# Performance work log

Measured on AMD Instinct MI355X. Metric: run time of the kernel, lower is better.

## Reference

```python
import jax, jax.numpy as jnp
import numpy as np
from jax import lax

T, LC = 4096, 20           # sentence length, max word length in chars
CV, CE, CO = 100, 25, 25   # char vocab, char emb dim, char-cnn out channels
V, E = 100000, 512         # word vocab, word emb dim
H = 1024                   # lstm hidden size per direction
NT, START, STOP = 12, 10, 11
NEG = -10000.0


def _lstm_dir(x, w_ih, w_hh, b_ih, b_hh):
    # x: [T, In] -> hs: [T, H]; pytorch gate order i, f, g, o
    pre = x @ w_ih.T + (b_ih + b_hh)              # [T, 4H] (input part hoisted out of scan)
    h0 = jnp.zeros((H,), x.dtype)
    def step(carry, p):
        h, c = carry
        g = p + h @ w_hh.T
        i, f, gg, o = jnp.split(g, 4)
        i = jax.nn.sigmoid(i); f = jax.nn.sigmoid(f)
        gg = jnp.tanh(gg); o = jax.nn.sigmoid(o)
        c = f * c + i * gg
        h = o * jnp.tanh(c)
        return (h, c), h
    _, hs = lax.scan(step, (h0, h0), pre)
    return hs


def _features(sentence, chars, char_emb, cnn_w, cnn_b, word_emb,
              w_ih_f, w_hh_f, b_ih_f, b_hh_f, w_ih_b, w_hh_b, b_ih_b, b_hh_b,
              w_tag, b_tag):
    # char CNN: embed -> conv2d(kernel (3,CE), pad (2,0)) -> max-pool over full time axis
    ce = char_emb[chars][:, None, :, :]            # [T,1,LC,CE]
    y = lax.conv_general_dilated(ce, cnn_w, (1, 1), ((2, 2), (0, 0)),
                                 dimension_numbers=('NCHW', 'OIHW', 'NCHW'))
    y = y + cnn_b[None, :, None, None]             # [T,CO,LC+2,1]
    char_feat = y.max(axis=(2, 3))                 # [T,CO]
    emb = jnp.concatenate([word_emb[sentence], char_feat], axis=1)  # [T,E+CO]
    # dropout is identity in eval mode
    hf = _lstm_dir(emb, w_ih_f, w_hh_f, b_ih_f, b_hh_f)
    hb = _lstm_dir(emb[::-1], w_ih_b, w_hh_b, b_ih_b, b_hh_b)[::-1]
    out = jnp.concatenate([hf, hb], axis=1)        # [T,2H]
    return out @ w_tag.T + b_tag                   # [T,NT]


def _viterbi(feats, transitions):
    alpha0 = jnp.full((NT,), NEG, feats.dtype).at[START].set(0.0)
    def step(alpha, feat):
        smat = alpha[:, None] + feat[None, :] + transitions   # [from, to]
        return jax.nn.logsumexp(smat, axis=0), jnp.argmax(smat, axis=0)
    alpha, bptrs = lax.scan(step, alpha0, feats)               # bptrs: [T,NT]
    final = alpha + transitions[:, STOP]                       # [NT]
    score = jax.nn.logsumexp(final)
    best_last = jnp.argmax(final)
    def back(best, b):
        nb = b[best]
        return nb, nb
    _, prev = lax.scan(back, best_last, bptrs[1:][::-1])
    path = jnp.concatenate([prev[::-1], best_last[None]])      # [T]
    return score, path


def setup_inputs() -> dict:
    key = jax.random.key(0)
    ks = jax.random.split(key, 18)
    IN = E + CO
    tr = jax.random.normal(ks[17], (NT, NT), jnp.float32)
    tr = tr.at[:, START].set(NEG).at[STOP, :].set(NEG)
    return {
        'sentence': jax.random.randint(ks[0], (T,), 0, V),
        'chars': jax.random.randint(ks[1], (T, LC), 0, CV),
        'caps': jax.random.randint(ks[2], (T,), 0, 4),
        'char_emb': jax.random.normal(ks[3], (CV, CE), jnp.float32),
        'cnn_w': jax.random.normal(ks[4], (CO, 1, 3, CE), jnp.float32) * 0.1,
        'cnn_b': jax.random.normal(ks[5], (CO,), jnp.float32) * 0.1,
        'word_emb': jax.random.normal(ks[6], (V, E), jnp.float32),
        'w_ih_f': jax.random.normal(ks[7], (4 * H, IN), jnp.float32) * 0.02,
        'w_hh_f': jax.random.normal(ks[8], (4 * H, H), jnp.float32) * 0.02,
        'b_ih_f': jax.random.normal(ks[9], (4 * H,), jnp.float32) * 0.02,
        'b_hh_f': jax.random.normal(ks[10], (4 * H,), jnp.float32) * 0.02,
        'w_ih_b': jax.random.normal(ks[11], (4 * H, IN), jnp.float32) * 0.02,
        'w_hh_b': jax.random.normal(ks[12], (4 * H, H), jnp.float32) * 0.02,
        'b_ih_b': jax.random.normal(ks[13], (4 * H,), jnp.float32) * 0.02,
        'b_hh_b': jax.random.normal(ks[14], (4 * H,), jnp.float32) * 0.02,
        'w_tag': jax.random.normal(ks[15], (NT, 2 * H), jnp.float32) * 0.02,
        'b_tag': jax.random.normal(ks[16], (NT,), jnp.float32) * 0.02,
        'transitions': tr,
    }


def reference(sentence, chars, caps, char_emb, cnn_w, cnn_b, word_emb,
              w_ih_f, w_hh_f, b_ih_f, b_hh_f, w_ih_b, w_hh_b, b_ih_b, b_hh_b,
              w_tag, b_tag, transitions):
    # caps is accepted by the original forward signature but never used
    feats = _features(sentence, chars, char_emb, cnn_w, cnn_b, word_emb,
                      w_ih_f, w_hh_f, b_ih_f, b_hh_f, w_ih_b, w_hh_b,
                      b_ih_b, b_hh_b, w_tag, b_tag)
    return _viterbi(feats, transitions)
```

## Files before the change

### kernel.cpp

```cpp
#include <hip/hip_runtime.h>
#include <math.h>


#define T_LEN 4096
#define NTAG 12
#define START_TAG 10
#define STOP_TAG 11
#define NEG_VAL (-10000.0f)

typedef int   v4i __attribute__((ext_vector_type(4)));
typedef float v4f __attribute__((ext_vector_type(4)));
typedef short sh8 __attribute__((ext_vector_type(8)));
typedef float f32x4 __attribute__((ext_vector_type(4)));

#define OF_EMB  0UL
#define OF_W    (OF_EMB + 4096UL * 544UL)
#define OF_BIAS (OF_W + 8192UL * 544UL)
#define OF_PRE  (OF_BIAS + 8192UL)
#define OF_HF   (OF_PRE + 4096UL * 8192UL)
#define OF_HB   (OF_HF + 4097UL * 1024UL)
#define OF_FEAT (OF_HB + 4097UL * 1024UL)

__device__ __forceinline__ float fsig(float v) {
    return 1.0f / (1.0f + __expf(-v));
}
__device__ __forceinline__ float ftanhf(float v) {
    float a = fabsf(v);
    float e = __expf(-2.0f * a);
    float r = (1.0f - e) / (1.0f + e);
    return copysignf(r, v);
}
__device__ __forceinline__ unsigned f2bf(float x) {
    unsigned u = __float_as_uint(x);
    u += 0x7fffu + ((u >> 16) & 1u);
    return u >> 16;
}

__global__ void prep_w_kernel(const float* __restrict__ wf, const float* __restrict__ wb,
                              const float* __restrict__ bif, const float* __restrict__ bhf,
                              const float* __restrict__ bib, const float* __restrict__ bhb,
                              unsigned short* __restrict__ wbf, float* __restrict__ bias) {
    int n = blockIdx.x;
    const float* src = (n < 4096) ? (wf + (size_t)n * 537) : (wb + (size_t)(n - 4096) * 537);
    unsigned short* dst = wbf + (size_t)n * 544;
    for (int k = threadIdx.x; k < 544; k += blockDim.x)
        dst[k] = (k < 537) ? (unsigned short)f2bf(src[k]) : (unsigned short)0;
    if (threadIdx.x == 0)
        bias[n] = (n < 4096) ? (bif[n] + bhf[n]) : (bib[n - 4096] + bhb[n - 4096]);
}

__global__ void charcnn_kernel(const int* __restrict__ sentence, const int* __restrict__ chars,
                               const float* __restrict__ cemb, const float* __restrict__ cw,
                               const float* __restrict__ cb, const float* __restrict__ wemb,
                               unsigned short* __restrict__ emb) {
    int t = blockIdx.x, tid = threadIdx.x;
    __shared__ float ce[500];
    __shared__ float yv[550];
    for (int i = tid; i < 500; i += 256) {
        int c = chars[t * 20 + i / 25];
        ce[i] = cemb[c * 25 + i % 25];
    }
    __syncthreads();
    for (int i = tid; i < 550; i += 256) {
        int o = i / 22, p = i % 22;
        float v = cb[o];
        #pragma unroll
        for (int kh = 0; kh < 3; ++kh) {
            int ir = p - 2 + kh;
            if (ir >= 0 && ir < 20) {
                const float* crow = ce + ir * 25;
                const float* wrow = cw + o * 75 + kh * 25;
                #pragma unroll
                for (int kw = 0; kw < 25; ++kw) v = fmaf(crow[kw], wrow[kw], v);
            }
        }
        yv[o * 22 + p] = v;
    }
    __syncthreads();
    unsigned short* erow = emb + (size_t)t * 544;
    int sidx = sentence[t];
    if (tid < 128) {
        float4 v = ((const float4*)(wemb + (size_t)sidx * 512))[tid];
        uint2 pk;
        pk.x = f2bf(v.x) | (f2bf(v.y) << 16);
        pk.y = f2bf(v.z) | (f2bf(v.w) << 16);
        ((uint2*)erow)[tid] = pk;
    }
    if (tid >= 128 && tid < 153) {
        int o = tid - 128;
        const float* yo = yv + o * 22;
        float m = yo[0];
        #pragma unroll
        for (int p = 1; p < 22; ++p) m = fmaxf(m, yo[p]);
        erow[512 + o] = (unsigned short)f2bf(m);
    }
    if (tid >= 160 && tid < 167) erow[537 + (tid - 160)] = 0;
}

__global__ __launch_bounds__(256) void sgemm_kernel(const unsigned short* __restrict__ A,
                                                    const unsigned short* __restrict__ B,
                                                    const float* __restrict__ bias,
                                                    float* __restrict__ C) {
    __shared__ unsigned short As[128 * 40];
    __shared__ unsigned short Bs[128 * 40];
    const int tid = threadIdx.x;
    const int wv = tid >> 6, lane = tid & 63;
    const int l15 = lane & 15, l4 = lane >> 4;
    const int m0 = blockIdx.y * 128, n0 = blockIdx.x * 128;
    const int srow = tid >> 2, sslot = tid & 3;

    f32x4 acc[2][8];
    #pragma unroll
    for (int mt = 0; mt < 2; ++mt)
        #pragma unroll
        for (int nt = 0; nt < 8; ++nt) acc[mt][nt] = (f32x4){0.f, 0.f, 0.f, 0.f};

    for (int kt = 0; kt < 17; ++kt) {
        const int kof = kt * 32 + sslot * 8;
        uint4 a0 = *(const uint4*)(A + (size_t)(m0 + srow) * 544 + kof);
        uint4 a1 = *(const uint4*)(A + (size_t)(m0 + 64 + srow) * 544 + kof);
        uint4 b0 = *(const uint4*)(B + (size_t)(n0 + srow) * 544 + kof);
        uint4 b1 = *(const uint4*)(B + (size_t)(n0 + 64 + srow) * 544 + kof);
        __syncthreads();
        *(uint4*)&As[srow * 40 + sslot * 8] = a0;
        *(uint4*)&As[(64 + srow) * 40 + sslot * 8] = a1;
        *(uint4*)&Bs[srow * 40 + sslot * 8] = b0;
        *(uint4*)&Bs[(64 + srow) * 40 + sslot * 8] = b1;
        __syncthreads();
        sh8 bfr[8];
        #pragma unroll
        for (int nt = 0; nt < 8; ++nt)
            bfr[nt] = *(const sh8*)&Bs[(16 * nt + l15) * 40 + l4 * 8];
        #pragma unroll
        for (int mt = 0; mt < 2; ++mt) {
            sh8 afr = *(const sh8*)&As[(32 * wv + 16 * mt + l15) * 40 + l4 * 8];
            #pragma unroll
            for (int nt = 0; nt < 8; ++nt)
                acc[mt][nt] = __builtin_amdgcn_mfma_f32_16x16x32_bf16(
                    afr, bfr[nt], acc[mt][nt], 0, 0, 0);
        }
    }
    #pragma unroll
    for (int mt = 0; mt < 2; ++mt) {
        int mrow = m0 + 32 * wv + 16 * mt + l4 * 4;
        #pragma unroll
        for (int nt = 0; nt < 8; ++nt) {
            int col = n0 + 16 * nt + l15;
            float bz = bias[col];
            #pragma unroll
            for (int r = 0; r < 4; ++r)
                C[(size_t)(mrow + r) * 8192 + col] = acc[mt][nt][r] + bz;
        }
    }
}

__global__ __launch_bounds__(512, 2) void lstm_kernel(const float* __restrict__ whhf,
                                                      const float* __restrict__ whhb,
                                                      const float* __restrict__ pre,
                                                      float* __restrict__ hfbuf,
                                                      float* __restrict__ hbbuf) {
    const int tid = threadIdx.x;
    const int dir = blockIdx.x >> 6;
    const int widx = blockIdx.x & 63;
    const int j0 = widx * 16;
    const int c32 = tid >> 4;
    const int r4 = tid & 15;
    const int lane = tid & 63;
    const int wv = tid >> 6;
    const bool pol = (r4 < 8);
    __shared__ __align__(16) float partials[2][8][64];

    v4f w[4][8];
    #pragma unroll
    for (int i = 0; i < 4; ++i) {
        int R = 4 * r4 + i;
        const v4f* wsrc = (const v4f*)((dir ? whhb : whhf) +
            (size_t)(((R >> 4) << 10) + j0 + (R & 15)) * 1024 + c32 * 32);
        #pragma unroll
        for (int m = 0; m < 8; ++m) w[i][m] = wsrc[m];
    }
    #pragma unroll
    for (int i = 0; i < 4; ++i)
        #pragma unroll
        for (int m = 0; m < 8; ++m)
            asm volatile("" : "+v"(w[i][m]));

    float* hbuf = dir ? hbbuf : hfbuf;
    const int dirofs = dir ? 4096 : 0;
    float c = 0.f;

    for (int s = 0; s < T_LEN; ++s) {
        const int t = dir ? (T_LEN - 1 - s) : s;
        const int rdslot = dir ? (t + 1) : t;
        const int wrslot = dir ? t : (t + 1);
        const int p = s & 1;

        float preg = 0.f;
        if (tid < 64)
            preg = pre[(size_t)t * 8192 + dirofs + ((lane & 3) << 10) + j0 + (lane >> 2)];

        const float* hp = hbuf + ((size_t)rdslot << 10) + c32 * 32 + r4 * 4;
        v4i hq;
        hq.x = 0; hq.y = 0; hq.z = 0; hq.w = 0;
        if (pol) {
            asm volatile("global_load_dwordx4 %0, %1, off sc1\n\ts_waitcnt vmcnt(0)"
                         : "=v"(hq) : "v"(hp));
        }
        while (true) {
            bool miss = pol && (hq.x == -1 || hq.y == -1 || hq.z == -1 || hq.w == -1);
            if (!__any(miss)) break;
            __builtin_amdgcn_s_sleep(1);
            if (miss) {
                asm volatile("global_load_dwordx4 %0, %1, off sc1\n\ts_waitcnt vmcnt(0)"
                             : "=v"(hq) : "v"(hp));
            }
        }

        float a0 = 0.f, a1 = 0.f, a2 = 0.f, a3 = 0.f;
        #pragma unroll
        for (int m = 0; m < 8; ++m) {
            int src = (lane & 48) + m;
            float hx = __shfl(__int_as_float(hq.x), src);
            float hy = __shfl(__int_as_float(hq.y), src);
            float hz = __shfl(__int_as_float(hq.z), src);
            float hw = __shfl(__int_as_float(hq.w), src);
            a0 = fmaf(w[0][m].x, hx, a0); a0 = fmaf(w[0][m].y, hy, a0);
            a0 = fmaf(w[0][m].z, hz, a0); a0 = fmaf(w[0][m].w, hw, a0);
            a1 = fmaf(w[1][m].x, hx, a1); a1 = fmaf(w[1][m].y, hy, a1);
            a1 = fmaf(w[1][m].z, hz, a1); a1 = fmaf(w[1][m].w, hw, a1);
            a2 = fmaf(w[2][m].x, hx, a2); a2 = fmaf(w[2][m].y, hy, a2);
            a2 = fmaf(w[2][m].z, hz, a2); a2 = fmaf(w[2][m].w, hw, a2);
            a3 = fmaf(w[3][m].x, hx, a3); a3 = fmaf(w[3][m].y, hy, a3);
            a3 = fmaf(w[3][m].z, hz, a3); a3 = fmaf(w[3][m].w, hw, a3);
        }
        a0 += __shfl_xor(a0, 16); a0 += __shfl_xor(a0, 32);
        a1 += __shfl_xor(a1, 16); a1 += __shfl_xor(a1, 32);
        a2 += __shfl_xor(a2, 16); a2 += __shfl_xor(a2, 32);
        a3 += __shfl_xor(a3, 16); a3 += __shfl_xor(a3, 32);
        if ((lane >> 4) == 0)
            *(float4*)&partials[p][wv][r4 << 2] = make_float4(a0, a1, a2, a3);
        __syncthreads();

        if (tid < 64) {
            int rql = ((lane & 3) << 4) + (lane >> 2);
            float dsum = 0.f;
            #pragma unroll
            for (int q = 0; q < 8; ++q) dsum += partials[p][q][rql];
            float val = preg + dsum;
            float act = ((lane & 3) == 2) ? ftanhf(val) : fsig(val);
            int base = lane & ~3;
            float iv = __shfl(act, base);
            float fv = __shfl(act, base + 1);
            float gv = __shfl(act, base + 2);
            float ov = __shfl(act, base + 3);
            c = fv * c + iv * gv;
            float h = ov * ftanhf(c);
            v4f hv;
            hv.x = __shfl(h, (lane << 4) & 63);
            hv.y = __shfl(h, ((lane << 4) + 4) & 63);
            hv.z = __shfl(h, ((lane << 4) + 8) & 63);
            hv.w = __shfl(h, ((lane << 4) + 12) & 63);
            if (lane < 4) {
                float* hp2 = hbuf + ((size_t)wrslot << 10) + j0 + (lane << 2);
                asm volatile("global_store_dwordx4 %0, %1, off sc1"
                             :: "v"(hp2), "v"(hv));
            }
        }
    }
}

__global__ __launch_bounds__(192) void tagproj_kernel(const float* __restrict__ hfbuf,
                                                      const float* __restrict__ hbbuf,
                                                      const float* __restrict__ wtag,
                                                      const float* __restrict__ btag,
                                                      float* __restrict__ feats) {
    int t = blockIdx.x, tid = threadIdx.x;
    __shared__ float4 hs4[512];
    for (int i = tid; i < 512; i += 192) {
        float4 q = (i < 256)
            ? ((const float4*)(hfbuf + ((size_t)(t + 1) << 10)))[i]
            : ((const float4*)(hbbuf + ((size_t)t << 10)))[i - 256];
        hs4[i ^ ((i >> 5) & 7)] = q;
    }
    __syncthreads();
    int tag = tid >> 4, sl = tid & 15;
    const float4* wrow4 = (const float4*)(wtag + (size_t)tag * 2048 + (sl << 7));
    float a = 0.f;
    #pragma unroll
    for (int m = 0; m < 32; ++m) {
        float4 h4 = hs4[(sl << 5) + (m ^ (sl & 7))];
        float4 w4 = wrow4[m];
        a = fmaf(h4.x, w4.x, a);
        a = fmaf(h4.y, w4.y, a);
        a = fmaf(h4.z, w4.z, a);
        a = fmaf(h4.w, w4.w, a);
    }
    a += __shfl_xor(a, 1);
    a += __shfl_xor(a, 2);
    a += __shfl_xor(a, 4);
    a += __shfl_xor(a, 8);
    if (sl == 0) feats[t * 12 + tag] = a + btag[tag];
}

__global__ __launch_bounds__(64) void viterbi_kernel(const float* __restrict__ feats,
                                                     const float* __restrict__ trans,
                                                     float* __restrict__ out) {
    const int tid = threadIdx.x;
    __shared__ float fbuf[256 * 12];
    __shared__ unsigned char bp[4096 * 12];
    float trf[12];
    float alpha = NEG_VAL;
    float tstop = 0.f;
    if (tid < 12) {
        #pragma unroll
        for (int f = 0; f < 12; ++f) trf[f] = trans[f * 12 + tid];
        if (tid == START_TAG) alpha = 0.f;
        tstop = trans[tid * 12 + STOP_TAG];
    }
    for (int ck = 0; ck < 16; ++ck) {
        __syncthreads();
        for (int i = tid; i < 3072; i += 64) fbuf[i] = feats[ck * 3072 + i];
        __syncthreads();
        if (tid < 12) {
            for (int tt = 0; tt < 256; ++tt) {
                float feat = fbuf[tt * 12 + tid];
                float sv[12];
                float m = -INFINITY;
                int best = 0;
                #pragma unroll
                for (int f = 0; f < 12; ++f) {
                    float af = __shfl(alpha, f);
                    float s = (af + feat) + trf[f];
                    sv[f] = s;
                    if (s > m) { m = s; best = f; }
                }
                float sum = 0.f;
                #pragma unroll
                for (int f = 0; f < 12; ++f) sum += __expf(sv[f] - m);
                alpha = __logf(sum) + m;
                bp[(ck * 256 + tt) * 12 + tid] = (unsigned char)best;
            }
        }
    }
    if (tid < 12) {
        float fin = alpha + tstop;
        float m = -INFINITY;
        int bl = 0;
        #pragma unroll
        for (int f = 0; f < 12; ++f) {
            float vf = __shfl(fin, f);
            if (vf > m) { m = vf; bl = f; }
        }
        float sum = 0.f;
        #pragma unroll
        for (int f = 0; f < 12; ++f) {
            float vf = __shfl(fin, f);
            sum += __expf(vf - m);
        }
        float score = __logf(sum) + m;
        if (tid == 0) {
            out[0] = score;
            out[4096] = (float)bl;
        }
        int cur = bl;
        for (int tt = 4095; tt >= 1; --tt) {
            int bv = (int)bp[tt * 12 + tid];
            cur = __shfl(bv, cur);
            if (tid == 0) out[tt] = (float)cur;
        }
    }
}

extern "C" void kernel_launch(void* const* d_in, const int* in_sizes, int n_in,
                              void* d_out, int out_size, void* d_ws, size_t ws_size,
                              hipStream_t stream) {
    (void)in_sizes; (void)n_in; (void)out_size; (void)ws_size;
    const int* sentence = (const int*)d_in[0];
    const int* chars = (const int*)d_in[1];
    const float* cemb = (const float*)d_in[3];
    const float* cw = (const float*)d_in[4];
    const float* cb = (const float*)d_in[5];
    const float* wemb = (const float*)d_in[6];
    const float* w_ih_f = (const float*)d_in[7];
    const float* w_hh_f = (const float*)d_in[8];
    const float* b_ih_f = (const float*)d_in[9];
    const float* b_hh_f = (const float*)d_in[10];
    const float* w_ih_b = (const float*)d_in[11];
    const float* w_hh_b = (const float*)d_in[12];
    const float* b_ih_b = (const float*)d_in[13];
    const float* b_hh_b = (const float*)d_in[14];
    const float* wtag = (const float*)d_in[15];
    const float* btag = (const float*)d_in[16];
    const float* trans = (const float*)d_in[17];

    float* ws = (float*)d_ws;
    unsigned short* emb_bf = (unsigned short*)(ws + OF_EMB);
    unsigned short* w_bf = (unsigned short*)(ws + OF_W);
    float* bias = ws + OF_BIAS;
    float* pre = ws + OF_PRE;
    float* hf = ws + OF_HF;
    float* hb = ws + OF_HB;
    float* feats = ws + OF_FEAT;

    (void)hipMemsetAsync(hf, 0xFF, 4097UL * 1024UL * 4UL, stream);
    (void)hipMemsetAsync(hb, 0xFF, 4097UL * 1024UL * 4UL, stream);
    (void)hipMemsetAsync(hf, 0x00, 1024UL * 4UL, stream);
    (void)hipMemsetAsync(hb + 4096UL * 1024UL, 0x00, 1024UL * 4UL, stream);

    hipLaunchKernelGGL(prep_w_kernel, dim3(8192), dim3(256), 0, stream,
                       w_ih_f, w_ih_b, b_ih_f, b_hh_f, b_ih_b, b_hh_b, w_bf, bias);
    hipLaunchKernelGGL(charcnn_kernel, dim3(4096), dim3(256), 0, stream,
                       sentence, chars, cemb, cw, cb, wemb, emb_bf);
    hipLaunchKernelGGL(sgemm_kernel, dim3(64, 32), dim3(256), 0, stream,
                       emb_bf, w_bf, bias, pre);
    hipLaunchKernelGGL(lstm_kernel, dim3(128), dim3(512), 0, stream,
                       w_hh_f, w_hh_b, pre, hf, hb);
    hipLaunchKernelGGL(tagproj_kernel, dim3(4096), dim3(192), 0, stream,
                       hf, hb, wtag, btag, feats);
    hipLaunchKernelGGL(viterbi_kernel, dim3(1), dim3(64), 0, stream,
                       feats, trans, (float*)d_out);
}
```

Measured before the change: 11.09 ms.

## Split Viterbi from-state reduction across four lane groups with shuffle reductions

The Viterbi recurrence now uses all 64 lanes: each group of 16 lanes handles three of the twelve 'from' states for each 'to' tag. Partial max/argmax and logsumexp values are combined across groups with xor shuffles. This shortens the per-step serial chain of twelve shuffles and exps on the critical path, but adds cross-lane shuffle reduction latency at every step.

```diff
diff --git a/kernel.cpp b/kernel.cpp
--- a/kernel.cpp
+++ b/kernel.cpp
@@ -306,42 +306,48 @@
                                                      const float* __restrict__ trans,
                                                      float* __restrict__ out) {
     const int tid = threadIdx.x;
+    const int q = tid >> 4;
+    const int to = tid & 15;
+    const int toc = (to < 12) ? to : 11;
     __shared__ float fbuf[256 * 12];
     __shared__ unsigned char bp[4096 * 12];
-    float trf[12];
-    float alpha = NEG_VAL;
-    float tstop = 0.f;
-    if (tid < 12) {
-        #pragma unroll
-        for (int f = 0; f < 12; ++f) trf[f] = trans[f * 12 + tid];
-        if (tid == START_TAG) alpha = 0.f;
-        tstop = trans[tid * 12 + STOP_TAG];
-    }
+
+    const float trf0 = trans[(3 * q + 0) * 12 + toc];
+    const float trf1 = trans[(3 * q + 1) * 12 + toc];
+    const float trf2 = trans[(3 * q + 2) * 12 + toc];
+    const float tstop = (tid < 12) ? trans[tid * 12 + STOP_TAG] : 0.f;
+    float alpha = (tid == START_TAG) ? 0.f : NEG_VAL;
+
     for (int ck = 0; ck < 16; ++ck) {
         __syncthreads();
         for (int i = tid; i < 3072; i += 64) fbuf[i] = feats[ck * 3072 + i];
         __syncthreads();
-        if (tid < 12) {
-            for (int tt = 0; tt < 256; ++tt) {
-                float feat = fbuf[tt * 12 + tid];
-                float sv[12];
-                float m = -INFINITY;
-                int best = 0;
-                #pragma unroll
-                for (int f = 0; f < 12; ++f) {
-                    float af = __shfl(alpha, f);
-                    float s = (af + feat) + trf[f];
-                    sv[f] = s;
-                    if (s > m) { m = s; best = f; }
-                }
-                float sum = 0.f;
-                #pragma unroll
-                for (int f = 0; f < 12; ++f) sum += __expf(sv[f] - m);
-                alpha = __logf(sum) + m;
-                bp[(ck * 256 + tt) * 12 + tid] = (unsigned char)best;
-            }
-        }
-    }
+        for (int tt = 0; tt < 256; ++tt) {
+            float feat = fbuf[tt * 12 + toc];
+            float af0 = __shfl(alpha, 3 * q + 0);
+            float af1 = __shfl(alpha, 3 * q + 1);
+            float af2 = __shfl(alpha, 3 * q + 2);
+            float s0 = (af0 + feat) + trf0;
+            float s1 = (af1 + feat) + trf1;
+            float s2 = (af2 + feat) + trf2;
+            float m = s0; int bi = 3 * q;
+            if (s1 > m) { m = s1; bi = 3 * q + 1; }
+            if (s2 > m) { m = s2; bi = 3 * q + 2; }
+            float mo = __shfl_xor(m, 16);
+            int io = __shfl_xor(bi, 16);
+            if (!((m > mo) || (m == mo && bi < io))) { m = mo; bi = io; }
+            mo = __shfl_xor(m, 32);
+            io = __shfl_xor(bi, 32);
+            if (!((m > mo) || (m == mo && bi < io))) { m = mo; bi = io; }
+            float e = __expf(s0 - m) + __expf(s1 - m) + __expf(s2 - m);
+            e += __shfl_xor(e, 16);
+            e += __shfl_xor(e, 32);
+            alpha = __logf(e) + m;
+            if (q == 0 && to < 12)
+                bp[(ck * 256 + tt) * 12 + to] = (unsigned char)bi;
+        }
+    }
+    __syncthreads();
     if (tid < 12) {
         float fin = alpha + tstop;
         float m = -INFINITY;
```

Result: faster. 10.72 ms, median of 2 (-3.4%).
